# Optimization experiments

Measured on AMD Instinct MI355X. Metric: run time of the kernel, lower is better.

The kernel has to match this reference:

```python
import jax, jax.numpy as jnp
import numpy as np

D = 768      # num_hiddens (hardcoded by dense1/dense2/ln in the source)
H = 12       # num_heads
NEG = -1000000.0
EPS = 1e-5


def setup_inputs() -> dict:
    key = jax.random.key(0)
    ks = jax.random.split(key, 14)
    B, Lq, Lk = 8, 1024, 1024
    s = 0.02
    return {
        "queries": jax.random.normal(ks[0], (B, Lq, D), dtype=jnp.float32),
        "keys":    jax.random.normal(ks[1], (B, Lk, D), dtype=jnp.float32),
        "values":  jax.random.normal(ks[2], (B, Lk, D), dtype=jnp.float32),
        # binary padding masks; count_nonzero along axis 1 gives valid lens
        "mask_1": jax.random.randint(ks[3], (B, Lk), 0, 2, dtype=jnp.int32),
        "mask_2": jax.random.randint(ks[4], (B, Lq), 0, 2, dtype=jnp.int32),
        # projection weights stored as [in, out] (torch Linear is y = x @ W.T)
        "Wq": jax.random.normal(ks[5], (D, D), dtype=jnp.float32) * s,
        "Wk": jax.random.normal(ks[6], (D, D), dtype=jnp.float32) * s,
        "Wv": jax.random.normal(ks[7], (D, D), dtype=jnp.float32) * s,
        "Wo": jax.random.normal(ks[8], (D, D), dtype=jnp.float32) * s,
        "d1_w": jax.random.normal(ks[9], (D, D), dtype=jnp.float32) * s,
        "d1_b": jnp.zeros((D,), dtype=jnp.float32),
        "d2_w": jax.random.normal(ks[10], (D, D), dtype=jnp.float32) * s,
        "d2_b": jnp.zeros((D,), dtype=jnp.float32),
        "ln_g": jnp.ones((D,), dtype=jnp.float32),
        "ln_b": jnp.zeros((D,), dtype=jnp.float32),
    }


def _cross_att(queries, keys, values, mask_1, mask_2,
               Wq, Wk, Wv, Wo, d1_w, d1_b, d2_w, d2_b, ln_g, ln_b):
    B, Lq, _ = queries.shape
    Lk = keys.shape[1]
    hd = D // H
    # project + split heads: [B, H, L, hd]
    q = (queries @ Wq).reshape(B, Lq, H, hd).transpose(0, 2, 1, 3)
    k = (keys    @ Wk).reshape(B, Lk, H, hd).transpose(0, 2, 1, 3)
    v = (values  @ Wv).reshape(B, Lk, H, hd).transpose(0, 2, 1, 3)
    scores = jnp.einsum('bhqd,bhkd->bhqk', q, k) / jnp.sqrt(jnp.float32(hd))
    # dual-axis prefix mask from nonzero counts
    vl1 = jnp.sum(mask_1 != 0, axis=1)  # [B], masks key axis
    vl2 = jnp.sum(mask_2 != 0, axis=1)  # [B], masks query axis
    col_ok = jnp.arange(Lk)[None, None, None, :] < vl1[:, None, None, None]
    row_ok = jnp.arange(Lq)[None, None, :, None] < vl2[:, None, None, None]
    scores = jnp.where(col_ok & row_ok, scores, NEG)
    attn = jax.nn.softmax(scores, axis=-1)
    out = jnp.einsum('bhqk,bhkd->bhqd', attn, v)
    out = out.transpose(0, 2, 1, 3).reshape(B, Lq, D)
    mha = out @ Wo
    ffn = jax.nn.relu(mha @ d1_w + d1_b) @ d2_w + d2_b
    x = ffn + mha  # dropout is identity in eval
    mu = jnp.mean(x, axis=-1, keepdims=True)
    var = jnp.mean(jnp.square(x - mu), axis=-1, keepdims=True)
    return (x - mu) / jnp.sqrt(var + EPS) * ln_g + ln_b


def reference(queries, keys, values, mask_1, mask_2,
              Wq, Wk, Wv, Wo, d1_w, d1_b, d2_w, d2_b, ln_g, ln_b):
    return _cross_att(queries, keys, values, mask_1, mask_2,
                      Wq, Wk, Wv, Wo, d1_w, d1_b, d2_w, d2_b, ln_g, ln_b)
```

## Files before the change

kernel.cpp:

```cpp
#include <hip/hip_runtime.h>
#include <hip/hip_bf16.h>
#include <type_traits>

#define DM   768
#define NH   12
#define HD   64
#define BATCH 8
#define SEQ  1024
#define NROWS (BATCH * SEQ)

typedef short bf16x8 __attribute__((ext_vector_type(8)));
typedef float f32x4 __attribute__((ext_vector_type(4)));

__device__ inline unsigned short f2b(float x) {
    union { float f; unsigned int u; } v; v.f = x;
    return (unsigned short)((v.u + 0x8000u) >> 16);
}
__device__ inline unsigned int f2b2(float lo, float hi) {
    union { float f; unsigned int u; } a, b; a.f = lo; b.f = hi;
    return __builtin_amdgcn_perm(b.u + 0x8000u, a.u + 0x8000u, 0x07060302u);
}
__device__ inline float b2f(unsigned short u) {
    union { float f; unsigned int x; } v; v.x = ((unsigned int)u) << 16;
    return v.f;
}

__device__ inline void gld16(const unsigned short* g, unsigned short* l) {
    __builtin_amdgcn_global_load_lds(
        (const __attribute__((address_space(1))) unsigned int*)g,
        (__attribute__((address_space(3))) unsigned int*)l, 16, 0, 0);
}

__global__ __launch_bounds__(256) void prep_kernel(const float* __restrict__ w0,
                                                   const float* __restrict__ w1,
                                                   const float* __restrict__ w2,
                                                   const float* __restrict__ w3,
                                                   const float* __restrict__ w4,
                                                   const float* __restrict__ w5,
                                                   unsigned short* __restrict__ wt,
                                                   const int* __restrict__ m1,
                                                   const int* __restrict__ m2,
                                                   int* __restrict__ lens,
                                                   const float* __restrict__ qin,
                                                   const float* __restrict__ kin,
                                                   const float* __restrict__ vin,
                                                   unsigned short* __restrict__ oq,
                                                   unsigned short* __restrict__ ok,
                                                   unsigned short* __restrict__ ov) {
    const int z = blockIdx.z;
    const int t = threadIdx.x;

    if (z >= 7) {
        const int linear = (z - 7) * 576 + blockIdx.y * 24 + blockIdx.x;
        const int g = linear / 3072;
        const int r = linear % 3072;
        const float* src = (g == 0) ? qin : (g == 1) ? kin : vin;
        unsigned short* dst = (g == 0) ? oq : (g == 1) ? ok : ov;
        const size_t i = ((size_t)r * 256 + t) * 8;
        float4 f0 = ((const float4*)(src + i))[0];
        float4 f1 = ((const float4*)(src + i))[1];
        uint4 p;
        p.x = f2b2(f0.x, f0.y); p.y = f2b2(f0.z, f0.w);
        p.z = f2b2(f1.x, f1.y); p.w = f2b2(f1.z, f1.w);
        *(uint4*)(dst + i) = p;
        return;
    }

    if (z < 6) {
        __shared__ float tile[32][33];
        const float* W = (z == 0) ? w0 : (z == 1) ? w1 : (z == 2) ? w2
                       : (z == 3) ? w3 : (z == 4) ? w4 : w5;
        unsigned short* Wt = wt + (size_t)z * DM * DM;
        const int n0 = blockIdx.x * 32;
        const int k0 = blockIdx.y * 32;
        const int tx = t & 31;
        const int ty = t >> 5;
#pragma unroll
        for (int r = 0; r < 4; ++r)
            tile[ty + 8 * r][tx] = W[(size_t)(k0 + ty + 8 * r) * DM + n0 + tx];
        __syncthreads();
#pragma unroll
        for (int r = 0; r < 4; ++r)
            Wt[(size_t)(n0 + ty + 8 * r) * DM + k0 + tx] = f2b(tile[tx][ty + 8 * r]);
        return;
    }

    if (blockIdx.y == 12) {
        if (blockIdx.x >= 16) return;
        __shared__ int redi[256];
        const int bid = blockIdx.x;
        const int b = bid & 7;
        const int* m = (bid < 8) ? m1 : m2;
        int cnt = 0;
        for (int i = t; i < SEQ; i += 256) cnt += (m[b * SEQ + i] != 0) ? 1 : 0;
        redi[t] = cnt;
        __syncthreads();
        for (int off = 128; off > 0; off >>= 1) {
            if (t < off) redi[t] += redi[t + off];
            __syncthreads();
        }
        if (t == 0) lens[bid] = redi[0];
        return;
    }

    if (blockIdx.x >= 12 || blockIdx.y >= 12) return;
    {
        __shared__ __align__(16) unsigned short As[64][40];
        __shared__ __align__(16) unsigned short Bs[64][40];
        unsigned short* out = wt + (size_t)6 * DM * DM;
        const float* Wo = w3;
        const float* d1w = w4;
        const int mb = blockIdx.x * 64;
        const int nb = blockIdx.y * 64;
        const int wid = t >> 6, lane = t & 63;
        const int quad = lane >> 4, l16 = lane & 15;
        const int bk = t >> 3, bn = (t & 7) * 8;
        const int am = t >> 2, ak = (t & 3) * 8;

        f32x4 acc[4];
#pragma unroll
        for (int c = 0; c < 4; ++c) acc[c] = (f32x4){0.f, 0.f, 0.f, 0.f};

        for (int j0 = 0; j0 < DM; j0 += 32) {
            {
                const float* s = &d1w[(size_t)(j0 + bk) * DM + mb + bn];
                float4 f0 = ((const float4*)s)[0];
                float4 f1 = ((const float4*)s)[1];
                As[bn + 0][bk] = f2b(f0.x); As[bn + 1][bk] = f2b(f0.y);
                As[bn + 2][bk] = f2b(f0.z); As[bn + 3][bk] = f2b(f0.w);
                As[bn + 4][bk] = f2b(f1.x); As[bn + 5][bk] = f2b(f1.y);
                As[bn + 6][bk] = f2b(f1.z); As[bn + 7][bk] = f2b(f1.w);
            }
            {
                const float* s = &Wo[(size_t)(nb + am) * DM + j0 + ak];
                float4 f0 = ((const float4*)s)[0];
                float4 f1 = ((const float4*)s)[1];
                uint4 p;
                p.x = f2b2(f0.x, f0.y); p.y = f2b2(f0.z, f0.w);
                p.z = f2b2(f1.x, f1.y); p.w = f2b2(f1.z, f1.w);
                *(uint4*)&Bs[am][ak] = p;
            }
            __syncthreads();
            bf16x8 av = *(const bf16x8*)&As[16 * wid + l16][quad * 8];
#pragma unroll
            for (int c = 0; c < 4; ++c) {
                bf16x8 bv = *(const bf16x8*)&Bs[16 * c + l16][quad * 8];
                acc[c] = __builtin_amdgcn_mfma_f32_16x16x32_bf16(av, bv, acc[c], 0, 0, 0);
            }
            __syncthreads();
        }
#pragma unroll
        for (int c = 0; c < 4; ++c) {
            const int col = nb + 16 * c + l16;
#pragma unroll
            for (int r = 0; r < 4; ++r) {
                const int row = mb + 16 * wid + quad * 4 + r;
                out[(size_t)row * DM + col] = f2b(acc[c][r]);
            }
        }
    }
}

__global__ __launch_bounds__(256) void qkv_gemm(const unsigned short* __restrict__ aq,
                                                const unsigned short* __restrict__ akk,
                                                const unsigned short* __restrict__ av_,
                                                const unsigned short* __restrict__ wt,
                                                unsigned short* __restrict__ c0,
                                                unsigned short* __restrict__ c1,
                                                unsigned short* __restrict__ c2) {
    __shared__ __align__(16) unsigned short As[128][32];
    __shared__ __align__(16) unsigned short Ws[128][32];

    const int t = threadIdx.x;
    const int g = blockIdx.y / 6;
    const int m0 = blockIdx.x * 128;
    const int n0 = (blockIdx.y % 6) * 128;
    const unsigned short* A = (g == 0) ? aq : (g == 1) ? akk : av_;
    const unsigned short* Wt = wt + (size_t)g * DM * DM;
    unsigned short* C = (g == 0) ? c0 : (g == 1) ? c1 : c2;
    const float cs = (g == 0) ? 0.18033688f : 1.0f;

    const int w = t >> 6, lane = t & 63;
    const int quad = lane >> 4, l16 = lane & 15;
    const int wm = w & 1, wn = w >> 1;
    const int srow = 16 * w + (lane >> 2);
    const int scol = 8 * (lane & 3);

    f32x4 acc[4][4];
#pragma unroll
    for (int i = 0; i < 4; ++i)
#pragma unroll
        for (int j = 0; j < 4; ++j) acc[i][j] = (f32x4){0.f, 0.f, 0.f, 0.f};

    for (int k0 = 0; k0 < DM; k0 += 32) {
#pragma unroll
        for (int j = 0; j < 2; ++j) {
            gld16(&A[(size_t)(m0 + srow + 64 * j) * DM + k0 + scol],
                  &As[16 * w + 64 * j][0]);
            gld16(&Wt[(size_t)(n0 + srow + 64 * j) * DM + k0 + scol],
                  &Ws[16 * w + 64 * j][0]);
        }
        __syncthreads();

        bf16x8 av[4], bv[4];
#pragma unroll
        for (int i = 0; i < 4; ++i)
            av[i] = *(const bf16x8*)&As[wm * 64 + 16 * i + l16][quad * 8];
#pragma unroll
        for (int i = 0; i < 4; ++i)
            bv[i] = *(const bf16x8*)&Ws[wn * 64 + 16 * i + l16][quad * 8];
#pragma unroll
        for (int i = 0; i < 4; ++i)
#pragma unroll
            for (int j = 0; j < 4; ++j)
                acc[i][j] = __builtin_amdgcn_mfma_f32_16x16x32_bf16(av[i], bv[j], acc[i][j], 0, 0, 0);
        __syncthreads();
    }

#pragma unroll
    for (int i = 0; i < 4; ++i)
#pragma unroll
        for (int j = 0; j < 4; ++j) {
            const int gn = n0 + wn * 64 + 16 * j + l16;
#pragma unroll
            for (int r = 0; r < 4; ++r) {
                const int gm = m0 + wm * 64 + 16 * i + quad * 4 + r;
                C[(size_t)gm * DM + gn] = f2b(acc[i][j][r] * cs);
            }
        }
}

template <typename CT>
__global__ __launch_bounds__(256) void gemm_bf(const unsigned short* __restrict__ A,
                                               const unsigned short* __restrict__ Wt,
                                               CT* __restrict__ C,
                                               const float* __restrict__ bias,
                                               const unsigned short* __restrict__ res,
                                               int relu) {
    __shared__ __align__(16) unsigned short As[128][32];
    __shared__ __align__(16) unsigned short Ws[128][32];

    const int t = threadIdx.x;
    const int m0 = blockIdx.x * 128;
    const int n0 = blockIdx.y * 128;
    const int w = t >> 6, lane = t & 63;
    const int quad = lane >> 4, l16 = lane & 15;
    const int wm = w & 1, wn = w >> 1;
    const int srow = 16 * w + (lane >> 2);
    const int scol = 8 * (lane & 3);

    f32x4 acc[4][4];
#pragma unroll
    for (int i = 0; i < 4; ++i)
#pragma unroll
        for (int j = 0; j < 4; ++j) acc[i][j] = (f32x4){0.f, 0.f, 0.f, 0.f};

    for (int k0 = 0; k0 < DM; k0 += 32) {
#pragma unroll
        for (int j = 0; j < 2; ++j) {
            gld16(&A[(size_t)(m0 + srow + 64 * j) * DM + k0 + scol],
                  &As[16 * w + 64 * j][0]);
            gld16(&Wt[(size_t)(n0 + srow + 64 * j) * DM + k0 + scol],
                  &Ws[16 * w + 64 * j][0]);
        }
        __syncthreads();

        bf16x8 av[4], bv[4];
#pragma unroll
        for (int i = 0; i < 4; ++i)
            av[i] = *(const bf16x8*)&As[wm * 64 + 16 * i + l16][quad * 8];
#pragma unroll
        for (int i = 0; i < 4; ++i)
            bv[i] = *(const bf16x8*)&Ws[wn * 64 + 16 * i + l16][quad * 8];
#pragma unroll
        for (int i = 0; i < 4; ++i)
#pragma unroll
            for (int j = 0; j < 4; ++j)
                acc[i][j] = __builtin_amdgcn_mfma_f32_16x16x32_bf16(av[i], bv[j], acc[i][j], 0, 0, 0);
        __syncthreads();
    }

#pragma unroll
    for (int i = 0; i < 4; ++i)
#pragma unroll
        for (int j = 0; j < 4; ++j) {
            const int gn = n0 + wn * 64 + 16 * j + l16;
            const float badd = bias ? bias[gn] : 0.0f;
#pragma unroll
            for (int r = 0; r < 4; ++r) {
                const int gm = m0 + wm * 64 + 16 * i + quad * 4 + r;
                float cv = acc[i][j][r] + badd;
                if (relu) cv = fmaxf(cv, 0.0f);
                if (res) cv += b2f(res[(size_t)gm * DM + gn]);
                if constexpr (std::is_same<CT, float>::value) {
                    C[(size_t)gm * DM + gn] = cv;
                } else {
                    C[(size_t)gm * DM + gn] = f2b(cv);
                }
            }
        }
}

__global__ __launch_bounds__(256) void gemm_mh(const unsigned short* __restrict__ A,
                                               const unsigned short* __restrict__ wt,
                                               unsigned short* __restrict__ cm,
                                               unsigned short* __restrict__ ch,
                                               const float* __restrict__ d1b) {
    __shared__ __align__(16) unsigned short As[128][32];
    __shared__ __align__(16) unsigned short Ws[128][32];

    const int t = threadIdx.x;
    const int unit = blockIdx.y / 6;
    const unsigned short* Wt = wt + (size_t)(unit ? 6 : 3) * DM * DM;
    unsigned short* C = unit ? ch : cm;
    const int m0 = blockIdx.x * 128;
    const int n0 = (blockIdx.y % 6) * 128;
    const int w = t >> 6, lane = t & 63;
    const int quad = lane >> 4, l16 = lane & 15;
    const int wm = w & 1, wn = w >> 1;
    const int srow = 16 * w + (lane >> 2);
    const int scol = 8 * (lane & 3);

    f32x4 acc[4][4];
#pragma unroll
    for (int i = 0; i < 4; ++i)
#pragma unroll
        for (int j = 0; j < 4; ++j) acc[i][j] = (f32x4){0.f, 0.f, 0.f, 0.f};

    for (int k0 = 0; k0 < DM; k0 += 32) {
#pragma unroll
        for (int j = 0; j < 2; ++j) {
            gld16(&A[(size_t)(m0 + srow + 64 * j) * DM + k0 + scol],
                  &As[16 * w + 64 * j][0]);
            gld16(&Wt[(size_t)(n0 + srow + 64 * j) * DM + k0 + scol],
                  &Ws[16 * w + 64 * j][0]);
        }
        __syncthreads();

        bf16x8 av[4], bv[4];
#pragma unroll
        for (int i = 0; i < 4; ++i)
            av[i] = *(const bf16x8*)&As[wm * 64 + 16 * i + l16][quad * 8];
#pragma unroll
        for (int i = 0; i < 4; ++i)
            bv[i] = *(const bf16x8*)&Ws[wn * 64 + 16 * i + l16][quad * 8];
#pragma unroll
        for (int i = 0; i < 4; ++i)
#pragma unroll
            for (int j = 0; j < 4; ++j)
                acc[i][j] = __builtin_amdgcn_mfma_f32_16x16x32_bf16(av[i], bv[j], acc[i][j], 0, 0, 0);
        __syncthreads();
    }

#pragma unroll
    for (int i = 0; i < 4; ++i)
#pragma unroll
        for (int j = 0; j < 4; ++j) {
            const int gn = n0 + wn * 64 + 16 * j + l16;
            const float badd = unit ? d1b[gn] : 0.0f;
#pragma unroll
            for (int r = 0; r < 4; ++r) {
                const int gm = m0 + wm * 64 + 16 * i + quad * 4 + r;
                float cv = acc[i][j][r] + badd;
                if (unit) cv = fmaxf(cv, 0.0f);
                C[(size_t)gm * DM + gn] = f2b(cv);
            }
        }
}

__global__ __launch_bounds__(256) void attn_mfma(const unsigned short* Q,
                                                 const unsigned short* __restrict__ K,
                                                 const unsigned short* __restrict__ V,
                                                 unsigned short* O,
                                                 const int* __restrict__ lens) {
    __shared__ __align__(16) unsigned short Ks[64][72];
    __shared__ __align__(16) unsigned short Vt[64][72];
    __shared__ __align__(16) unsigned short Ps[4][16][72];

    const int t = threadIdx.x;
    const int bid = blockIdx.x;
    const int q0 = (bid & 15) * 64;
    const int h = (bid >> 4) % NH;
    const int b = bid / (16 * NH);
    const int vl1 = lens[b];
    const int vl2 = lens[8 + b];
    const int wid = t >> 6;
    const int lane = t & 63;
    const int quad = lane >> 4;
    const int l16 = lane & 15;

    bf16x8 qa0, qa1;
    {
        const unsigned short* qp =
            &Q[(size_t)(b * SEQ + q0 + 16 * wid + l16) * DM + h * HD + quad * 8];
        qa0 = *(const bf16x8*)qp;
        qa1 = *(const bf16x8*)(qp + 32);
    }

    f32x4 o[4];
#pragma unroll
    for (int ct = 0; ct < 4; ++ct) o[ct] = (f32x4){0.f, 0.f, 0.f, 0.f};
    float suml[4];
    bool rbad[4];
#pragma unroll
    for (int r = 0; r < 4; ++r) {
        suml[r] = 0.0f;
        rbad[r] = ((q0 + 16 * wid + quad * 4 + r) >= vl2) || (vl1 == 0);
    }

    const int kkr = t >> 3;
    const int khc = (t & 7) * 8;
    const unsigned short* kbase = &K[(size_t)(b * SEQ) * DM + h * HD];
    const unsigned short* vbase = &V[(size_t)(b * SEQ) * DM + h * HD];

    uint4 kr0 = *(const uint4*)&kbase[(size_t)kkr * DM + khc];
    uint4 kr1 = *(const uint4*)&kbase[(size_t)(kkr + 32) * DM + khc];
    uint4 vr0 = *(const uint4*)&vbase[(size_t)lane * DM + wid * 16];
    uint4 vr1 = *(const uint4*)&vbase[(size_t)lane * DM + wid * 16 + 8];

    const int k2 = l16 >> 2;

    for (int tile = 0; tile < 16; ++tile) {
        const int c0 = tile * 64;
        *(uint4*)&Ks[kkr][khc] = kr0;
        *(uint4*)&Ks[kkr + 32][khc] = kr1;
        {
            union { uint4 u; unsigned short s[8]; } va, vb;
            va.u = vr0; vb.u = vr1;
#pragma unroll
            for (int j = 0; j < 8; ++j) Vt[wid * 16 + j][lane] = va.s[j];
#pragma unroll
            for (int j = 0; j < 8; ++j) Vt[wid * 16 + 8 + j][lane] = vb.s[j];
        }
        __syncthreads();

        if (tile < 15) {
            const int c1 = c0 + 64;
            kr0 = *(const uint4*)&kbase[(size_t)(c1 + kkr) * DM + khc];
            kr1 = *(const uint4*)&kbase[(size_t)(c1 + kkr + 32) * DM + khc];
            vr0 = *(const uint4*)&vbase[(size_t)(c1 + lane) * DM + wid * 16];
            vr1 = *(const uint4*)&vbase[(size_t)(c1 + lane) * DM + wid * 16 + 8];
        }

        f32x4 s[4];
#pragma unroll
        for (int ct = 0; ct < 4; ++ct) {
            f32x4 acc = (f32x4){0.f, 0.f, 0.f, 0.f};
            bf16x8 b0v = *(const bf16x8*)&Ks[16 * ct + l16][quad * 8];
            bf16x8 b1v = *(const bf16x8*)&Ks[16 * ct + l16][32 + quad * 8];
            acc = __builtin_amdgcn_mfma_f32_16x16x32_bf16(qa0, b0v, acc, 0, 0, 0);
            acc = __builtin_amdgcn_mfma_f32_16x16x32_bf16(qa1, b1v, acc, 0, 0, 0);
            s[ct] = acc;
        }
#pragma unroll
        for (int ct = 0; ct < 4; ++ct) {
            const bool kok = (c0 + 16 * ct + l16) < vl1;
#pragma unroll
            for (int r = 0; r < 4; ++r) {
                float e = exp2f(s[ct][r]);
                float p = kok ? e : 0.0f;
                p = rbad[r] ? 1.0f : p;
                s[ct][r] = p;
                suml[r] += p;
            }
        }
#pragma unroll
        for (int ct = 0; ct < 4; ++ct) {
            const int gidx = 2 * ct + (l16 >> 3);
            const int c = l16 & 7;
            const int gs = (gidx ^ quad) * 8 + c;
#pragma unroll
            for (int r = 0; r < 4; ++r)
                Ps[wid][quad * 4 + r][gs] = f2b(s[ct][r]);
        }
        bf16x8 pa0 = *(const bf16x8*)&Ps[wid][l16][(quad ^ k2) * 8];
        bf16x8 pa1 = *(const bf16x8*)&Ps[wid][l16][((4 + quad) ^ k2) * 8];
#pragma unroll
        for (int ct = 0; ct < 4; ++ct) {
            bf16x8 vb0 = *(const bf16x8*)&Vt[16 * ct + l16][quad * 8];
            bf16x8 vb1 = *(const bf16x8*)&Vt[16 * ct + l16][32 + quad * 8];
            o[ct] = __builtin_amdgcn_mfma_f32_16x16x32_bf16(pa0, vb0, o[ct], 0, 0, 0);
            o[ct] = __builtin_amdgcn_mfma_f32_16x16x32_bf16(pa1, vb1, o[ct], 0, 0, 0);
        }
        __syncthreads();
    }

#pragma unroll
    for (int d = 1; d < 16; d <<= 1) {
#pragma unroll
        for (int r = 0; r < 4; ++r) suml[r] += __shfl_xor(suml[r], d, 64);
    }
#pragma unroll
    for (int r = 0; r < 4; ++r) {
        float inv = 1.0f / suml[r];
        const size_t row = (size_t)(b * SEQ + q0 + 16 * wid + quad * 4 + r);
#pragma unroll
        for (int ct = 0; ct < 4; ++ct) {
            O[row * DM + h * HD + 16 * ct + l16] = f2b(o[ct][r] * inv);
        }
    }
}

__global__ __launch_bounds__(256) void ln_kernel(float* __restrict__ X,
                                                 const float* __restrict__ g,
                                                 const float* __restrict__ bvec) {
    __shared__ float red[256];
    const int row = blockIdx.x;
    const int t = threadIdx.x;
    float* xr = X + (size_t)row * DM;
    float x0 = xr[t];
    float x1 = xr[t + 256];
    float x2 = xr[t + 512];
    red[t] = x0 + x1 + x2;
    __syncthreads();
    for (int off = 128; off > 0; off >>= 1) {
        if (t < off) red[t] += red[t + off];
        __syncthreads();
    }
    float mu = red[0] * (1.0f / 768.0f);
    __syncthreads();
    float d0 = x0 - mu, d1 = x1 - mu, d2 = x2 - mu;
    red[t] = d0 * d0 + d1 * d1 + d2 * d2;
    __syncthreads();
    for (int off = 128; off > 0; off >>= 1) {
        if (t < off) red[t] += red[t + off];
        __syncthreads();
    }
    float rstd = rsqrtf(red[0] * (1.0f / 768.0f) + 1e-5f);
    xr[t]       = d0 * rstd * g[t]       + bvec[t];
    xr[t + 256] = d1 * rstd * g[t + 256] + bvec[t + 256];
    xr[t + 512] = d2 * rstd * g[t + 512] + bvec[t + 512];
}

extern "C" void kernel_launch(void* const* d_in, const int* in_sizes, int n_in,
                              void* d_out, int out_size, void* d_ws, size_t ws_size,
                              hipStream_t stream) {
    const float* queries = (const float*)d_in[0];
    const float* keys    = (const float*)d_in[1];
    const float* values  = (const float*)d_in[2];
    const int* mask1 = (const int*)d_in[3];
    const int* mask2 = (const int*)d_in[4];
    const float* Wq  = (const float*)d_in[5];
    const float* Wk  = (const float*)d_in[6];
    const float* Wv  = (const float*)d_in[7];
    const float* Wo  = (const float*)d_in[8];
    const float* d1w = (const float*)d_in[9];
    const float* d1b = (const float*)d_in[10];
    const float* d2w = (const float*)d_in[11];
    const float* d2b = (const float*)d_in[12];
    const float* lng = (const float*)d_in[13];
    const float* lnb = (const float*)d_in[14];

    char* ws = (char*)d_ws;
    int* lens = (int*)ws;
    const size_t NB = (size_t)NROWS * DM * sizeof(unsigned short);
    const size_t WT = (size_t)DM * DM;
    unsigned short* b0 = (unsigned short*)(ws + 256);
    unsigned short* b1 = (unsigned short*)(ws + 256 + NB);
    unsigned short* b2 = (unsigned short*)(ws + 256 + 2 * NB);
    unsigned short* wt = (unsigned short*)(ws + 256 + 3 * NB);
    unsigned short* aq = (unsigned short*)(ws + 256 + 3 * NB + 7 * WT * sizeof(unsigned short));
    unsigned short* ak = aq + (size_t)NROWS * DM;
    unsigned short* av = ak + (size_t)NROWS * DM;
    float* xout = (float*)d_out;

    prep_kernel<<<dim3(24, 24, 23), 256, 0, stream>>>(Wq, Wk, Wv, Wo, d1w, d2w,
                                                      wt, mask1, mask2, lens,
                                                      queries, keys, values,
                                                      aq, ak, av);

    qkv_gemm<<<dim3(64, 18), 256, 0, stream>>>(aq, ak, av, wt, b0, b1, b2);

    attn_mfma<<<16 * NH * BATCH, 256, 0, stream>>>(b0, b1, b2, b0, lens);

    gemm_mh<<<dim3(64, 12), 256, 0, stream>>>(b0, wt, b1, b2, d1b);

    gemm_bf<float><<<dim3(64, 6), 256, 0, stream>>>(b2, wt + 5 * WT, xout, d2b, b1, 0);

    ln_kernel<<<NROWS, 256, 0, stream>>>(xout, lng, lnb);
}
```

Baseline: 335.4 us.

## Skip masked key tiles and shortcut fully-masked query rows with precomputed V mean

Attention now loops only over key tiles up to the valid key length instead of all 16 tiles. Fully masked query rows, whose softmax is uniform, take their output from a per-(batch,head) mean of V. A new kernel precomputes that mean as partial sums, and blocks whose queries are all masked return early. This removes wasted MFMA and exp work on padded regions, at the cost of an extra small launch and a reordered workspace. The exp call is also swapped for the hardware builtin.

```diff
diff --git a/kernel.cpp b/kernel.cpp
--- a/kernel.cpp
+++ b/kernel.cpp
@@ -230,6 +230,25 @@
         }
 }
 
+__global__ __launch_bounds__(256) void vpart_kernel(const unsigned short* __restrict__ v,
+                                                    float* __restrict__ vp) {
+    __shared__ float red[4][64];
+    const int t = threadIdx.x;
+    const int bh = blockIdx.x;
+    const int chunk = blockIdx.y;
+    const int b = bh / NH, h = bh % NH;
+    const int d = t & 63, rg = t >> 6;
+    const unsigned short* base =
+        v + (size_t)(b * SEQ + chunk * 128 + rg * 32) * DM + h * HD + d;
+    float s = 0.0f;
+#pragma unroll 4
+    for (int i = 0; i < 32; ++i) s += b2f(base[(size_t)i * DM]);
+    red[rg][d] = s;
+    __syncthreads();
+    if (rg == 0)
+        vp[((size_t)bh * 8 + chunk) * 64 + d] = red[0][d] + red[1][d] + red[2][d] + red[3][d];
+}
+
 template <typename CT>
 __global__ __launch_bounds__(256) void gemm_bf(const unsigned short* __restrict__ A,
                                                const unsigned short* __restrict__ Wt,
@@ -372,7 +391,8 @@
                                                  const unsigned short* __restrict__ K,
                                                  const unsigned short* __restrict__ V,
                                                  unsigned short* O,
-                                                 const int* __restrict__ lens) {
+                                                 const int* __restrict__ lens,
+                                                 const float* __restrict__ vp) {
     __shared__ __align__(16) unsigned short Ks[64][72];
     __shared__ __align__(16) unsigned short Vt[64][72];
     __shared__ __align__(16) unsigned short Ps[4][16][72];
@@ -388,6 +408,26 @@
     const int lane = t & 63;
     const int quad = lane >> 4;
     const int l16 = lane & 15;
+    const size_t vpb = (size_t)(b * NH + h) * 8 * 64;
+
+    if (q0 >= vl2 || vl1 == 0) {
+        float vm[4];
+#pragma unroll
+        for (int ct = 0; ct < 4; ++ct) {
+            float s = 0.0f;
+#pragma unroll
+            for (int c = 0; c < 8; ++c) s += vp[vpb + (size_t)c * 64 + 16 * ct + l16];
+            vm[ct] = s * (1.0f / 1024.0f);
+        }
+#pragma unroll
+        for (int r = 0; r < 4; ++r) {
+            const size_t row = (size_t)(b * SEQ + q0 + 16 * wid + quad * 4 + r);
+#pragma unroll
+            for (int ct = 0; ct < 4; ++ct)
+                O[row * DM + h * HD + 16 * ct + l16] = f2b(vm[ct]);
+        }
+        return;
+    }
 
     bf16x8 qa0, qa1;
     {
@@ -405,8 +445,10 @@
 #pragma unroll
     for (int r = 0; r < 4; ++r) {
         suml[r] = 0.0f;
-        rbad[r] = ((q0 + 16 * wid + quad * 4 + r) >= vl2) || (vl1 == 0);
-    }
+        rbad[r] = (q0 + 16 * wid + quad * 4 + r) >= vl2;
+    }
+
+    const int nt = (vl1 + 63) >> 6;
 
     const int kkr = t >> 3;
     const int khc = (t & 7) * 8;
@@ -420,7 +462,7 @@
 
     const int k2 = l16 >> 2;
 
-    for (int tile = 0; tile < 16; ++tile) {
+    for (int tile = 0; tile < nt; ++tile) {
         const int c0 = tile * 64;
         *(uint4*)&Ks[kkr][khc] = kr0;
         *(uint4*)&Ks[kkr + 32][khc] = kr1;
@@ -434,7 +476,7 @@
         }
         __syncthreads();
 
-        if (tile < 15) {
+        if (tile < nt - 1) {
             const int c1 = c0 + 64;
             kr0 = *(const uint4*)&kbase[(size_t)(c1 + kkr) * DM + khc];
             kr1 = *(const uint4*)&kbase[(size_t)(c1 + kkr + 32) * DM + khc];
@@ -457,9 +499,8 @@
             const bool kok = (c0 + 16 * ct + l16) < vl1;
 #pragma unroll
             for (int r = 0; r < 4; ++r) {
-                float e = exp2f(s[ct][r]);
+                float e = __builtin_amdgcn_exp2f(s[ct][r]);
                 float p = kok ? e : 0.0f;
-                p = rbad[r] ? 1.0f : p;
                 s[ct][r] = p;
                 suml[r] += p;
             }
@@ -490,13 +531,25 @@
 #pragma unroll
         for (int r = 0; r < 4; ++r) suml[r] += __shfl_xor(suml[r], d, 64);
     }
+
+    float vm[4];
+    if (rbad[0] || rbad[3]) {
+#pragma unroll
+        for (int ct = 0; ct < 4; ++ct) {
+            float s = 0.0f;
+#pragma unroll
+            for (int c = 0; c < 8; ++c) s += vp[vpb + (size_t)c * 64 + 16 * ct + l16];
+            vm[ct] = s * (1.0f / 1024.0f);
+        }
+    }
 #pragma unroll
     for (int r = 0; r < 4; ++r) {
-        float inv = 1.0f / suml[r];
+        const float inv = 1.0f / suml[r];
         const size_t row = (size_t)(b * SEQ + q0 + 16 * wid + quad * 4 + r);
 #pragma unroll
         for (int ct = 0; ct < 4; ++ct) {
-            O[row * DM + h * HD + 16 * ct + l16] = f2b(o[ct][r] * inv);
+            const float val = rbad[r] ? vm[ct] : o[ct][r] * inv;
+            O[row * DM + h * HD + 16 * ct + l16] = f2b(val);
         }
     }
 }
@@ -553,13 +606,15 @@
 
     char* ws = (char*)d_ws;
     int* lens = (int*)ws;
+    float* vp = (float*)(ws + 256);
+    const size_t VP = (size_t)96 * 8 * 64 * sizeof(float);
     const size_t NB = (size_t)NROWS * DM * sizeof(unsigned short);
     const size_t WT = (size_t)DM * DM;
-    unsigned short* b0 = (unsigned short*)(ws + 256);
-    unsigned short* b1 = (unsigned short*)(ws + 256 + NB);
-    unsigned short* b2 = (unsigned short*)(ws + 256 + 2 * NB);
-    unsigned short* wt = (unsigned short*)(ws + 256 + 3 * NB);
-    unsigned short* aq = (unsigned short*)(ws + 256 + 3 * NB + 7 * WT * sizeof(unsigned short));
+    unsigned short* b0 = (unsigned short*)(ws + 256 + VP);
+    unsigned short* b1 = (unsigned short*)(ws + 256 + VP + NB);
+    unsigned short* b2 = (unsigned short*)(ws + 256 + VP + 2 * NB);
+    unsigned short* wt = (unsigned short*)(ws + 256 + VP + 3 * NB);
+    unsigned short* aq = (unsigned short*)(ws + 256 + VP + 3 * NB + 7 * WT * sizeof(unsigned short));
     unsigned short* ak = aq + (size_t)NROWS * DM;
     unsigned short* av = ak + (size_t)NROWS * DM;
     float* xout = (float*)d_out;
@@ -571,7 +626,9 @@
 
     qkv_gemm<<<dim3(64, 18), 256, 0, stream>>>(aq, ak, av, wt, b0, b1, b2);
 
-    attn_mfma<<<16 * NH * BATCH, 256, 0, stream>>>(b0, b1, b2, b0, lens);
+    vpart_kernel<<<dim3(96, 8), 256, 0, stream>>>(b2, vp);
+
+    attn_mfma<<<16 * NH * BATCH, 256, 0, stream>>>(b0, b1, b2, b0, lens, vp);
 
     gemm_mh<<<dim3(64, 12), 256, 0, stream>>>(b0, wt, b1, b2, d1b);
 
```

Result: faster. 316.9 us (-5.5%).
